# Kernel tuning notes

Hardware: AMD Instinct MI355X
Metric: run time of the kernel (lower is better)

Reference implementation:

```python
import jax, jax.numpy as jnp
import numpy as np

N_NODES = 50000
N_EDGES = 600000
IN_CH = 300
HID = 128
N_CLASSES = 2
N_GRAPHS = 128
BN_EPS = 1e-5


def setup_inputs() -> dict:
    key = jax.random.key(0)
    ks = jax.random.split(key, 24)
    x = jax.random.normal(ks[0], (N_NODES, IN_CH), dtype=jnp.float32)
    edge_index = jax.random.randint(ks[1], (2, N_EDGES), 0, N_NODES, dtype=jnp.int64)
    batch = jnp.sort(jax.random.randint(ks[2], (N_NODES,), 0, N_GRAPHS, dtype=jnp.int64))

    def glorot(k, shape):
        fan_in, fan_out = shape
        s = jnp.sqrt(2.0 / (fan_in + fan_out)).astype(jnp.float32)
        return jax.random.normal(k, shape, dtype=jnp.float32) * s

    inp = {"x": x, "edge_index": edge_index, "batch": batch}
    # SAGEConv params: W_l (neighbor branch), W_r (root branch), bias
    dims = [(IN_CH, HID), (HID, HID), (HID, HID)]
    for i, (din, dout) in enumerate(dims, start=1):
        inp[f"W{i}l"] = glorot(ks[3 * i], (din, dout))
        inp[f"W{i}r"] = glorot(ks[3 * i + 1], (din, dout))
        inp[f"b{i}"] = jnp.zeros((dout,), dtype=jnp.float32)
        inp[f"g{i}"] = jnp.ones((dout,), dtype=jnp.float32)   # BN gamma
        inp[f"be{i}"] = jnp.zeros((dout,), dtype=jnp.float32)  # BN beta
    inp["Wc"] = glorot(ks[20], (HID, N_CLASSES))
    inp["bc"] = jnp.zeros((N_CLASSES,), dtype=jnp.float32)
    return inp


def _sage_conv(x, src, dst, Wl, Wr, b):
    # mean-aggregate neighbor features (messages flow src -> dst)
    msg_sum = jax.ops.segment_sum(x[src], dst, num_segments=N_NODES)
    deg = jax.ops.segment_sum(jnp.ones((src.shape[0],), dtype=x.dtype), dst,
                              num_segments=N_NODES)
    mean = msg_sum / jnp.maximum(deg, 1.0)[:, None]
    return mean @ Wl + x @ Wr + b


def _bn_relu(h, gamma, beta):
    mu = jnp.mean(h, axis=0)
    var = jnp.var(h, axis=0)
    h = (h - mu) * jax.lax.rsqrt(var + BN_EPS) * gamma + beta
    return jax.nn.relu(h)


def reference(x, edge_index, batch,
              W1l, W1r, b1, g1, be1,
              W2l, W2r, b2, g2, be2,
              W3l, W3r, b3, g3, be3,
              Wc, bc):
    src, dst = edge_index[0], edge_index[1]
    h = _bn_relu(_sage_conv(x, src, dst, W1l, W1r, b1), g1, be1)
    h = _bn_relu(_sage_conv(h, src, dst, W2l, W2r, b2), g2, be2)
    h = _bn_relu(_sage_conv(h, src, dst, W3l, W3r, b3), g3, be3)
    # global mean pool per graph
    pooled = jax.ops.segment_sum(h, batch, num_segments=N_GRAPHS)
    cnt = jax.ops.segment_sum(jnp.ones((h.shape[0],), dtype=h.dtype), batch,
                              num_segments=N_GRAPHS)
    hg = pooled / jnp.maximum(cnt, 1.0)[:, None]
    out = hg @ Wc + bc
    return out, hg
```

## Files before the change

kernel.cpp:

```cpp
#include <hip/hip_runtime.h>

#define N_NODES   50000
#define N_EDGES   600000
#define IN_CH     300
#define HID       128
#define N_CLASSES 2
#define N_GRAPHS  128
#define BN_EPS    1e-5f

#define NB ((N_NODES + 511) / 512)
#define KP1 320
#define NREP 32

typedef __attribute__((ext_vector_type(8))) short bf8_t;
typedef __attribute__((ext_vector_type(4))) float f4_t;

__device__ __forceinline__ unsigned short f2bf(float x) {
    union { float f; unsigned u; } q; q.f = x;
    unsigned r = q.u + 0x7fffu + ((q.u >> 16) & 1u);
    return (unsigned short)(r >> 16);
}
__device__ __forceinline__ float bf2f(unsigned short h) {
    union { float f; unsigned u; } q; q.u = ((unsigned)h) << 16; return q.f;
}

__device__ __forceinline__ void async_cp16(const void* g, void* l) {
    __builtin_amdgcn_global_load_lds(
        (const __attribute__((address_space(1))) unsigned int*)g,
        (__attribute__((address_space(3))) unsigned int*)l, 16, 0, 0);
}

__global__ __launch_bounds__(256) void deg_kernel(const int* __restrict__ dst,
                                                  int* __restrict__ ideg) {
    int e = blockIdx.x * 256 + threadIdx.x;
    if (e < N_EDGES) atomicAdd(&ideg[dst[e]], 1);
}

__global__ __launch_bounds__(256) void scan_fused(const int* __restrict__ ideg,
                                                  int* __restrict__ row_start,
                                                  float* __restrict__ invdeg,
                                                  int* __restrict__ bsum,
                                                  int* __restrict__ bflag) {
    int b = blockIdx.x, t = threadIdx.x;
    int lane = t & 63, wv = t >> 6;
    int i0 = b * 512 + t * 2;
    int v0 = 0, v1 = 0;
    if (i0 < N_NODES) {
        int2 v = *(const int2*)&ideg[i0];
        v0 = v.x; v1 = v.y;
    }
    int tot = v0 + v1;
    int s = tot;
#pragma unroll
    for (int d = 1; d < 64; d <<= 1) {
        int u = __shfl_up(s, d);
        if (lane >= d) s += u;
    }
    __shared__ int ws[4];
    if (lane == 63) ws[wv] = s;
    __syncthreads();
    int btot = ws[0] + ws[1] + ws[2] + ws[3];
    if (t == 0) {
        atomicExch(&bsum[b], btot);
        __threadfence();
        atomicExch(&bflag[b], 1);
    }
    int part = 0;
    if (t < b) {
        while (atomicAdd(&bflag[t], 0) == 0) {}
        part = atomicAdd(&bsum[t], 0);
    }
#pragma unroll
    for (int d = 1; d < 64; d <<= 1) part += __shfl_down(part, d);
    __shared__ int ps[4];
    if (lane == 0) ps[wv] = part;
    __syncthreads();
    int boff = ps[0] + ps[1] + ps[2] + ps[3];
    int woff = 0;
    for (int w = 0; w < wv; ++w) woff += ws[w];
    int base = boff + woff + (s - tot);
    if (i0 < N_NODES) {
        row_start[i0]     = base;
        row_start[i0 + 1] = base + v0;
        invdeg[i0]     = 1.0f / fmaxf((float)v0, 1.0f);
        invdeg[i0 + 1] = 1.0f / fmaxf((float)v1, 1.0f);
    }
    if (t == 0 && b == NB - 1) row_start[N_NODES] = boff + btot;
}

__global__ __launch_bounds__(256) void fill_kernel(const int* __restrict__ src,
                                                   const int* __restrict__ dst,
                                                   const int* __restrict__ row_start,
                                                   int* __restrict__ cursor,
                                                   int* __restrict__ csr_src) {
    int e = blockIdx.x * 256 + threadIdx.x;
    if (e >= N_EDGES) return;
    int d = dst[e];
    int pos = row_start[d] + atomicAdd(&cursor[d], 1);
    csr_src[pos] = src[e];
}

__global__ __launch_bounds__(256) void prep_w_all(const float* __restrict__ W1l,
                                                  const float* __restrict__ W1r,
                                                  const float* __restrict__ W2l,
                                                  const float* __restrict__ W2r,
                                                  const float* __restrict__ W3l,
                                                  const float* __restrict__ W3r,
                                                  unsigned short* __restrict__ B1h,
                                                  unsigned short* __restrict__ B1l,
                                                  unsigned short* __restrict__ B2h,
                                                  unsigned short* __restrict__ B2l,
                                                  unsigned short* __restrict__ B3h,
                                                  unsigned short* __restrict__ B3l) {
    int layer = blockIdx.y;
    int Kp = (layer == 0) ? KP1 : HID;
    int K  = (layer == 0) ? IN_CH : HID;
    const float* Wl = (layer == 0) ? W1l : ((layer == 1) ? W2l : W3l);
    const float* Wr = (layer == 0) ? W1r : ((layer == 1) ? W2r : W3r);
    unsigned short* Bh = (layer == 0) ? B1h : ((layer == 1) ? B2h : B3h);
    unsigned short* Bl = (layer == 0) ? B1l : ((layer == 1) ? B2l : B3l);
    int idx = blockIdx.x * 256 + threadIdx.x;
    if (idx >= 256 * Kp) return;
    int n = idx / Kp;
    int k = idx - n * Kp;
    float v = 0.f;
    if (k < K) v = (n < 128) ? Wl[k * 128 + n] : Wr[k * 128 + (n - 128)];
    unsigned short h = f2bf(v);
    unsigned short l = f2bf(v - bf2f(h));
    Bh[idx] = h;
    Bl[idx] = l;
}

__global__ __launch_bounds__(256) void gemm_mfma(const unsigned short* __restrict__ Ahi,
                                                 const unsigned short* __restrict__ Alo,
                                                 int M, int Kp,
                                                 const unsigned short* __restrict__ Bhi,
                                                 const unsigned short* __restrict__ Blo,
                                                 const float* __restrict__ bias,
                                                 unsigned short* __restrict__ C0,
                                                 float* __restrict__ C1) {
    __shared__ __align__(16) unsigned short sAh[64 * 32];
    __shared__ __align__(16) unsigned short sAl[64 * 32];
    __shared__ __align__(16) unsigned short sBh[256 * 32];
    __shared__ __align__(16) unsigned short sBl[256 * 32];

    const int tid  = threadIdx.x;
    const int lane = tid & 63;
    const int wave = tid >> 6;
    const int l16  = lane & 15;
    const int quad = lane >> 4;
    const long m0  = (long)blockIdx.x * 64;
    const int  n0  = wave * 64;

    f4_t acc[4][4];
#pragma unroll
    for (int mt = 0; mt < 4; ++mt)
#pragma unroll
        for (int nt = 0; nt < 4; ++nt) acc[mt][nt] = (f4_t){0.f, 0.f, 0.f, 0.f};

    const int cg = ((lane & 3) ^ ((lane >> 3) & 3)) * 8;
    long asr = m0 + wave * 16 + (lane >> 2);
    if (asr >= M) asr = M - 1;
    const unsigned short* gAh = Ahi + asr * Kp + cg;
    const unsigned short* gAl = Alo + asr * Kp + cg;
    unsigned short* lAh = &sAh[wave * 512];
    unsigned short* lAl = &sAl[wave * 512];
    const unsigned short* gBh[4];
    const unsigned short* gBl[4];
    unsigned short* lBh[4];
    unsigned short* lBl[4];
#pragma unroll
    for (int j = 0; j < 4; ++j) {
        long br = wave * 64 + j * 16 + (lane >> 2);
        gBh[j] = Bhi + br * Kp + cg;
        gBl[j] = Blo + br * Kp + cg;
        lBh[j] = &sBh[wave * 2048 + j * 512];
        lBl[j] = &sBl[wave * 2048 + j * 512];
    }
    const int rsw = (quad ^ ((l16 >> 1) & 3)) * 8;

    for (int k0 = 0; k0 < Kp; k0 += 32) {
        async_cp16(gAh + k0, lAh);
        async_cp16(gAl + k0, lAl);
#pragma unroll
        for (int j = 0; j < 4; ++j) {
            async_cp16(gBh[j] + k0, lBh[j]);
            async_cp16(gBl[j] + k0, lBl[j]);
        }
        __syncthreads();

        bf8_t ah[4], al[4];
#pragma unroll
        for (int mt = 0; mt < 4; ++mt) {
            ah[mt] = *(const bf8_t*)&sAh[(mt * 16 + l16) * 32 + rsw];
            al[mt] = *(const bf8_t*)&sAl[(mt * 16 + l16) * 32 + rsw];
        }
#pragma unroll
        for (int nt = 0; nt < 4; ++nt) {
            bf8_t bh = *(const bf8_t*)&sBh[(n0 + nt * 16 + l16) * 32 + rsw];
            bf8_t bl = *(const bf8_t*)&sBl[(n0 + nt * 16 + l16) * 32 + rsw];
#pragma unroll
            for (int mt = 0; mt < 4; ++mt) {
                acc[mt][nt] = __builtin_amdgcn_mfma_f32_16x16x32_bf16(ah[mt], bh, acc[mt][nt], 0, 0, 0);
                acc[mt][nt] = __builtin_amdgcn_mfma_f32_16x16x32_bf16(al[mt], bh, acc[mt][nt], 0, 0, 0);
                acc[mt][nt] = __builtin_amdgcn_mfma_f32_16x16x32_bf16(ah[mt], bl, acc[mt][nt], 0, 0, 0);
            }
        }
        __syncthreads();
    }

    const bool left = (n0 < 128);
    if (left) {
        int ncol[4];
#pragma unroll
        for (int nt = 0; nt < 4; ++nt) ncol[nt] = n0 + nt * 16 + l16;
#pragma unroll
        for (int mt = 0; mt < 4; ++mt)
#pragma unroll
            for (int r = 0; r < 4; ++r) {
                long row = m0 + mt * 16 + quad * 4 + r;
                if (row < M) {
#pragma unroll
                    for (int nt = 0; nt < 4; ++nt)
                        C0[row * 128 + ncol[nt]] = f2bf(acc[mt][nt][r]);
                }
            }
    } else {
        float badd[4];
        int   ncol[4];
#pragma unroll
        for (int nt = 0; nt < 4; ++nt) {
            int ng = n0 + nt * 16 + l16 - 128;
            ncol[nt] = ng;
            badd[nt] = bias[ng];
        }
#pragma unroll
        for (int mt = 0; mt < 4; ++mt)
#pragma unroll
            for (int r = 0; r < 4; ++r) {
                long row = m0 + mt * 16 + quad * 4 + r;
                if (row < M) {
#pragma unroll
                    for (int nt = 0; nt < 4; ++nt)
                        C1[row * 128 + ncol[nt]] = acc[mt][nt][r] + badd[nt];
                }
            }
    }
}

__global__ __launch_bounds__(256) void gemm_mfma_x(const float* __restrict__ X,
                                                   int M,
                                                   const unsigned short* __restrict__ Bhi,
                                                   const unsigned short* __restrict__ Blo,
                                                   const float* __restrict__ bias,
                                                   unsigned short* __restrict__ C0,
                                                   float* __restrict__ C1) {
    __shared__ __align__(16) unsigned short sAh[64 * 32];
    __shared__ __align__(16) unsigned short sAl[64 * 32];
    __shared__ __align__(16) unsigned short sBh[256 * 32];
    __shared__ __align__(16) unsigned short sBl[256 * 32];

    const int tid  = threadIdx.x;
    const int lane = tid & 63;
    const int wave = tid >> 6;
    const int l16  = lane & 15;
    const int quad = lane >> 4;
    const long m0  = (long)blockIdx.x * 64;
    const int  n0  = wave * 64;

    f4_t acc[4][4];
#pragma unroll
    for (int mt = 0; mt < 4; ++mt)
#pragma unroll
        for (int nt = 0; nt < 4; ++nt) acc[mt][nt] = (f4_t){0.f, 0.f, 0.f, 0.f};

    const int ar  = tid >> 2;
    const int cl  = tid & 3;
    const int cpa = cl ^ ((ar >> 1) & 3);
    long agr = m0 + ar;
    if (agr >= M) agr = M - 1;
    const float* gX = X + agr * IN_CH;

    const int cg = ((lane & 3) ^ ((lane >> 3) & 3)) * 8;
    const unsigned short* gBh[4];
    const unsigned short* gBl[4];
    unsigned short* lBh[4];
    unsigned short* lBl[4];
#pragma unroll
    for (int j = 0; j < 4; ++j) {
        long br = wave * 64 + j * 16 + (lane >> 2);
        gBh[j] = Bhi + br * KP1 + cg;
        gBl[j] = Blo + br * KP1 + cg;
        lBh[j] = &sBh[wave * 2048 + j * 512];
        lBl[j] = &sBl[wave * 2048 + j * 512];
    }
    const int rsw = (quad ^ ((l16 >> 1) & 3)) * 8;

    for (int k0 = 0; k0 < KP1; k0 += 32) {
#pragma unroll
        for (int j = 0; j < 4; ++j) {
            async_cp16(gBh[j] + k0, lBh[j]);
            async_cp16(gBl[j] + k0, lBl[j]);
        }
        float f[8];
        const int gk = k0 + cl * 8;
#pragma unroll
        for (int hh = 0; hh < 2; ++hh) {
            int g4 = gk + hh * 4;
            float4 v = (g4 + 4 <= IN_CH) ? *(const float4*)(gX + g4)
                                         : make_float4(0.f, 0.f, 0.f, 0.f);
            f[hh * 4 + 0] = v.x; f[hh * 4 + 1] = v.y;
            f[hh * 4 + 2] = v.z; f[hh * 4 + 3] = v.w;
        }
        bf8_t h8, l8;
#pragma unroll
        for (int j = 0; j < 8; ++j) {
            unsigned short h = f2bf(f[j]);
            h8[j] = (short)h;
            l8[j] = (short)f2bf(f[j] - bf2f(h));
        }
        *(bf8_t*)&sAh[ar * 32 + cpa * 8] = h8;
        *(bf8_t*)&sAl[ar * 32 + cpa * 8] = l8;
        __syncthreads();

        bf8_t ah[4], al[4];
#pragma unroll
        for (int mt = 0; mt < 4; ++mt) {
            ah[mt] = *(const bf8_t*)&sAh[(mt * 16 + l16) * 32 + rsw];
            al[mt] = *(const bf8_t*)&sAl[(mt * 16 + l16) * 32 + rsw];
        }
#pragma unroll
        for (int nt = 0; nt < 4; ++nt) {
            bf8_t bh = *(const bf8_t*)&sBh[(n0 + nt * 16 + l16) * 32 + rsw];
            bf8_t bl = *(const bf8_t*)&sBl[(n0 + nt * 16 + l16) * 32 + rsw];
#pragma unroll
            for (int mt = 0; mt < 4; ++mt) {
                acc[mt][nt] = __builtin_amdgcn_mfma_f32_16x16x32_bf16(ah[mt], bh, acc[mt][nt], 0, 0, 0);
                acc[mt][nt] = __builtin_amdgcn_mfma_f32_16x16x32_bf16(al[mt], bh, acc[mt][nt], 0, 0, 0);
                acc[mt][nt] = __builtin_amdgcn_mfma_f32_16x16x32_bf16(ah[mt], bl, acc[mt][nt], 0, 0, 0);
            }
        }
        __syncthreads();
    }

    const bool left = (n0 < 128);
    if (left) {
        int ncol[4];
#pragma unroll
        for (int nt = 0; nt < 4; ++nt) ncol[nt] = n0 + nt * 16 + l16;
#pragma unroll
        for (int mt = 0; mt < 4; ++mt)
#pragma unroll
            for (int r = 0; r < 4; ++r) {
                long row = m0 + mt * 16 + quad * 4 + r;
                if (row < M) {
#pragma unroll
                    for (int nt = 0; nt < 4; ++nt)
                        C0[row * 128 + ncol[nt]] = f2bf(acc[mt][nt][r]);
                }
            }
    } else {
        float badd[4];
        int   ncol[4];
#pragma unroll
        for (int nt = 0; nt < 4; ++nt) {
            int ng = n0 + nt * 16 + l16 - 128;
            ncol[nt] = ng;
            badd[nt] = bias[ng];
        }
#pragma unroll
        for (int mt = 0; mt < 4; ++mt)
#pragma unroll
            for (int r = 0; r < 4; ++r) {
                long row = m0 + mt * 16 + quad * 4 + r;
                if (row < M) {
#pragma unroll
                    for (int nt = 0; nt < 4; ++nt)
                        C1[row * 128 + ncol[nt]] = acc[mt][nt][r] + badd[nt];
                }
            }
    }
}

__global__ __launch_bounds__(256) void gather_agg(const unsigned short* __restrict__ Pl,
                                                  const int* __restrict__ row_start,
                                                  const int* __restrict__ csr_src,
                                                  const float* __restrict__ invdeg,
                                                  float* __restrict__ out,
                                                  float* __restrict__ rep) {
    int slot = threadIdx.x >> 5;
    int lane = threadIdx.x & 31;
    int node = blockIdx.x * 8 + slot;
    int beg = row_start[node];
    int end = row_start[node + 1];
    const unsigned short* base = Pl + lane * 4;
    float sx = 0.f, sy = 0.f, sz = 0.f, sw = 0.f;
    int j = beg;
    for (; j + 8 <= end; j += 8) {
        int idx[8];
#pragma unroll
        for (int u = 0; u < 8; ++u) idx[u] = csr_src[j + u];
        ushort4 v[8];
#pragma unroll
        for (int u = 0; u < 8; ++u) v[u] = *(const ushort4*)(base + (long)idx[u] * HID);
#pragma unroll
        for (int u = 0; u < 8; ++u) {
            sx += bf2f(v[u].x); sy += bf2f(v[u].y);
            sz += bf2f(v[u].z); sw += bf2f(v[u].w);
        }
    }
    if (j + 4 <= end) {
        int idx[4];
#pragma unroll
        for (int u = 0; u < 4; ++u) idx[u] = csr_src[j + u];
        ushort4 v[4];
#pragma unroll
        for (int u = 0; u < 4; ++u) v[u] = *(const ushort4*)(base + (long)idx[u] * HID);
#pragma unroll
        for (int u = 0; u < 4; ++u) {
            sx += bf2f(v[u].x); sy += bf2f(v[u].y);
            sz += bf2f(v[u].z); sw += bf2f(v[u].w);
        }
        j += 4;
    }
    for (; j < end; ++j) {
        int i0 = csr_src[j];
        ushort4 v0 = *(const ushort4*)(base + (long)i0 * HID);
        sx += bf2f(v0.x); sy += bf2f(v0.y); sz += bf2f(v0.z); sw += bf2f(v0.w);
    }
    float w = invdeg[node];
    float* o = out + (long)node * HID + lane * 4;
    float4 cur = *(float4*)o;
    cur.x += sx * w;
    cur.y += sy * w;
    cur.z += sz * w;
    cur.w += sw * w;
    *(float4*)o = cur;

    __shared__ float red[8][HID];
    float* repb = rep + (blockIdx.x & (NREP - 1)) * 256;
    *(float4*)&red[slot][lane * 4] = make_float4(cur.x, cur.y, cur.z, cur.w);
    __syncthreads();
    if (threadIdx.x < HID) {
        float tsum = 0.f;
#pragma unroll
        for (int s = 0; s < 8; ++s) tsum += red[s][threadIdx.x];
        atomicAdd(&repb[threadIdx.x], tsum);
    }
    __syncthreads();
    *(float4*)&red[slot][lane * 4] = make_float4(cur.x * cur.x, cur.y * cur.y,
                                                 cur.z * cur.z, cur.w * cur.w);
    __syncthreads();
    if (threadIdx.x < HID) {
        float tsum = 0.f;
#pragma unroll
        for (int s = 0; s < 8; ++s) tsum += red[s][threadIdx.x];
        atomicAdd(&repb[HID + threadIdx.x], tsum);
    }
}

__global__ __launch_bounds__(256) void bn_apply_relu(float* __restrict__ h,
                                                     const float* __restrict__ rep,
                                                     const float* __restrict__ gamma,
                                                     const float* __restrict__ beta,
                                                     unsigned short* __restrict__ Hhi,
                                                     unsigned short* __restrict__ Hlo) {
    __shared__ float S[256];
    __shared__ float SC[256];
    int t = threadIdx.x;
    float a = 0.f;
#pragma unroll
    for (int r = 0; r < NREP; ++r) a += rep[r * 256 + t];
    S[t] = a;
    __syncthreads();
    if (t < HID) {
        const float invn = 1.0f / (float)N_NODES;
        float mu  = S[t] * invn;
        float var = S[HID + t] * invn - mu * mu;
        float sc  = gamma[t] * rsqrtf(var + BN_EPS);
        SC[t]       = sc;
        SC[HID + t] = beta[t] - mu * sc;
    }
    __syncthreads();

    long i = (long)blockIdx.x * 256 + t;
    if (i >= (long)N_NODES * 32) return;
    int c4 = (int)(i & 31) * 4;
    float4 sc = *(const float4*)&SC[c4];
    float4 sh = *(const float4*)&SC[HID + c4];
    float4 v  = *(float4*)&h[i * 4];
    v.x = fmaxf(v.x * sc.x + sh.x, 0.f);
    v.y = fmaxf(v.y * sc.y + sh.y, 0.f);
    v.z = fmaxf(v.z * sc.z + sh.z, 0.f);
    v.w = fmaxf(v.w * sc.w + sh.w, 0.f);
    if (Hhi) {
        ushort4 hh, ll;
        hh.x = f2bf(v.x); ll.x = f2bf(v.x - bf2f(hh.x));
        hh.y = f2bf(v.y); ll.y = f2bf(v.y - bf2f(hh.y));
        hh.z = f2bf(v.z); ll.z = f2bf(v.z - bf2f(hh.z));
        hh.w = f2bf(v.w); ll.w = f2bf(v.w - bf2f(hh.w));
        *(ushort4*)&Hhi[i * 4] = hh;
        *(ushort4*)&Hlo[i * 4] = ll;
    } else {
        *(float4*)&h[i * 4] = v;
    }
}

__global__ __launch_bounds__(1024) void poolhead_kernel(const float* __restrict__ h,
                                                        const int* __restrict__ batch,
                                                        const float* __restrict__ Wc,
                                                        const float* __restrict__ bc,
                                                        float* __restrict__ out) {
    int g = blockIdx.x;
    int t = threadIdx.x;
    int c = t & 127;
    int half = t >> 7;
    __shared__ int lo_sh, hi_sh;
    if (t == 0) {
        int lo = 0, hi = N_NODES;
        while (lo < hi) { int m = (lo + hi) >> 1; if (batch[m] < g) lo = m + 1; else hi = m; }
        lo_sh = lo;
        int lo2 = lo, hi2 = N_NODES;
        while (lo2 < hi2) { int m = (lo2 + hi2) >> 1; if (batch[m] < g + 1) lo2 = m + 1; else hi2 = m; }
        hi_sh = lo2;
    }
    __syncthreads();
    int lo = lo_sh, hi = hi_sh;
    float a0 = 0.f, a1 = 0.f, a2 = 0.f, a3 = 0.f;
    int r = lo + half;
    for (; r + 24 < hi; r += 32) {
        a0 += h[(long)(r +  0) * HID + c];
        a1 += h[(long)(r +  8) * HID + c];
        a2 += h[(long)(r + 16) * HID + c];
        a3 += h[(long)(r + 24) * HID + c];
    }
    for (; r < hi; r += 8) a0 += h[(long)r * HID + c];
    __shared__ float red[8][HID];
    red[half][c] = (a0 + a1) + (a2 + a3);
    __syncthreads();
    __shared__ float r0[HID], r1[HID];
    if (t < HID) {
        float inv = 1.0f / fmaxf((float)(hi - lo), 1.0f);
        float v = 0.f;
#pragma unroll
        for (int s = 0; s < 8; ++s) v += red[s][t];
        v *= inv;
        out[N_GRAPHS * N_CLASSES + g * HID + t] = v;
        r0[t] = v * Wc[t * 2 + 0];
        r1[t] = v * Wc[t * 2 + 1];
    }
    __syncthreads();
    if (t < 2) {
        const float* rr = t ? r1 : r0;
        float sum = bc[t];
        for (int i = 0; i < HID; ++i) sum += rr[i];
        out[g * 2 + t] = sum;
    }
}

extern "C" void kernel_launch(void* const* d_in, const int* in_sizes, int n_in,
                              void* d_out, int out_size, void* d_ws, size_t ws_size,
                              hipStream_t stream) {
    const float* x     = (const float*)d_in[0];
    const int*   ei    = (const int*)d_in[1];
    const int*   batch = (const int*)d_in[2];
    const float* W1l = (const float*)d_in[3];
    const float* W1r = (const float*)d_in[4];
    const float* b1  = (const float*)d_in[5];
    const float* g1  = (const float*)d_in[6];
    const float* be1 = (const float*)d_in[7];
    const float* W2l = (const float*)d_in[8];
    const float* W2r = (const float*)d_in[9];
    const float* b2  = (const float*)d_in[10];
    const float* g2  = (const float*)d_in[11];
    const float* be2 = (const float*)d_in[12];
    const float* W3l = (const float*)d_in[13];
    const float* W3r = (const float*)d_in[14];
    const float* b3  = (const float*)d_in[15];
    const float* g3  = (const float*)d_in[16];
    const float* be3 = (const float*)d_in[17];
    const float* Wc  = (const float*)d_in[18];
    const float* bc  = (const float*)d_in[19];

    const int* src = ei;
    const int* dst = ei + N_EDGES;

    float* ws = (float*)d_ws;
    const long FEAT = (long)N_NODES * HID;
    unsigned short* Pl16 = (unsigned short*)ws;
    float* buf1 = ws + FEAT;
    float* buf2 = ws + 2 * FEAT;
    int*   ideg      = (int*)(ws + 3 * FEAT);
    int*   cursor    = ideg + N_NODES;
    int*   bsum      = cursor + N_NODES;
    int*   bflag     = bsum + 128;
    int*   row_start = bflag + 128;
    int*   csr_src   = row_start + N_NODES + 4;
    float* invdeg    = (float*)(csr_src + N_EDGES);
    float* reps      = invdeg + N_NODES;
    unsigned short* B1h = (unsigned short*)(reps + 3 * NREP * 256);
    unsigned short* B1l = B1h + 256 * KP1;
    unsigned short* B2h = B1l + 256 * KP1;
    unsigned short* B2l = B2h + 256 * HID;
    unsigned short* B3h = B2l + 256 * HID;
    unsigned short* B3l = B3h + 256 * HID;
    unsigned short* Hhi = B3l + 256 * HID;
    unsigned short* Hlo = Hhi + FEAT;

    float* outp = (float*)d_out;

    const int gemm_grid   = (N_NODES + 63) / 64;
    const int gather_grid = N_NODES / 8;
    const int apply_grid  = (int)(((long)N_NODES * 32 + 255) / 256);
    const dim3 prepw_grid((256 * KP1 + 255) / 256, 3);

    hipMemsetAsync(ideg, 0, (2 * N_NODES + 256) * sizeof(int), stream);
    hipMemsetAsync(reps, 0, 3 * NREP * 256 * sizeof(float), stream);

    deg_kernel<<<(N_EDGES + 255) / 256, 256, 0, stream>>>(dst, ideg);
    scan_fused<<<NB, 256, 0, stream>>>(ideg, row_start, invdeg, bsum, bflag);
    fill_kernel<<<(N_EDGES + 255) / 256, 256, 0, stream>>>(src, dst, row_start, cursor, csr_src);

    prep_w_all<<<prepw_grid, 256, 0, stream>>>(W1l, W1r, W2l, W2r, W3l, W3r,
                                               B1h, B1l, B2h, B2l, B3h, B3l);

    gemm_mfma_x<<<gemm_grid, 256, 0, stream>>>(x, N_NODES, B1h, B1l, b1, Pl16, buf1);
    gather_agg<<<gather_grid, 256, 0, stream>>>(Pl16, row_start, csr_src, invdeg, buf1, reps);
    bn_apply_relu<<<apply_grid, 256, 0, stream>>>(buf1, reps, g1, be1, Hhi, Hlo);

    gemm_mfma<<<gemm_grid, 256, 0, stream>>>(Hhi, Hlo, N_NODES, HID, B2h, B2l, b2, Pl16, buf2);
    gather_agg<<<gather_grid, 256, 0, stream>>>(Pl16, row_start, csr_src, invdeg, buf2, reps + NREP * 256);
    bn_apply_relu<<<apply_grid, 256, 0, stream>>>(buf2, reps + NREP * 256, g2, be2, Hhi, Hlo);

    gemm_mfma<<<gemm_grid, 256, 0, stream>>>(Hhi, Hlo, N_NODES, HID, B3h, B3l, b3, Pl16, buf1);
    gather_agg<<<gather_grid, 256, 0, stream>>>(Pl16, row_start, csr_src, invdeg, buf1, reps + 2 * NREP * 256);
    bn_apply_relu<<<apply_grid, 256, 0, stream>>>(buf1, reps + 2 * NREP * 256, g3, be3, nullptr, nullptr);

    poolhead_kernel<<<N_GRAPHS, 1024, 0, stream>>>(buf1, batch, Wc, bc, outp);
}
```

Baseline: 443.6 us.

## Fuse BN+ReLU into next-layer GEMM A-load and pooling head; merge deg with weight prep

Result: faster. 399.2 us (-10.0%).

```diff
diff --git a/kernel.cpp b/kernel.cpp
--- a/kernel.cpp
+++ b/kernel.cpp
@@ -11,6 +11,7 @@
 #define NB ((N_NODES + 511) / 512)
 #define KP1 320
 #define NREP 32
+#define DEGB ((N_EDGES + 255) / 256)
 
 typedef __attribute__((ext_vector_type(8))) short bf8_t;
 typedef __attribute__((ext_vector_type(4))) float f4_t;
@@ -30,10 +31,46 @@
         (__attribute__((address_space(3))) unsigned int*)l, 16, 0, 0);
 }
 
-__global__ __launch_bounds__(256) void deg_kernel(const int* __restrict__ dst,
-                                                  int* __restrict__ ideg) {
-    int e = blockIdx.x * 256 + threadIdx.x;
-    if (e < N_EDGES) atomicAdd(&ideg[dst[e]], 1);
+__global__ __launch_bounds__(256) void deg_prepw(const int* __restrict__ dst,
+                                                 int* __restrict__ ideg,
+                                                 const float* __restrict__ W1l,
+                                                 const float* __restrict__ W1r,
+                                                 const float* __restrict__ W2l,
+                                                 const float* __restrict__ W2r,
+                                                 const float* __restrict__ W3l,
+                                                 const float* __restrict__ W3r,
+                                                 unsigned short* __restrict__ B1h,
+                                                 unsigned short* __restrict__ B1l,
+                                                 unsigned short* __restrict__ B2h,
+                                                 unsigned short* __restrict__ B2l,
+                                                 unsigned short* __restrict__ B3h,
+                                                 unsigned short* __restrict__ B3l) {
+    int b = blockIdx.x;
+    if (b < DEGB) {
+        int e = b * 256 + threadIdx.x;
+        if (e < N_EDGES) atomicAdd(&ideg[dst[e]], 1);
+        return;
+    }
+    int pb = b - DEGB;
+    int layer, base;
+    if (pb < 320)      { layer = 0; base = pb; }
+    else if (pb < 448) { layer = 1; base = pb - 320; }
+    else               { layer = 2; base = pb - 448; }
+    int Kp = (layer == 0) ? KP1 : HID;
+    int K  = (layer == 0) ? IN_CH : HID;
+    const float* Wl = (layer == 0) ? W1l : ((layer == 1) ? W2l : W3l);
+    const float* Wr = (layer == 0) ? W1r : ((layer == 1) ? W2r : W3r);
+    unsigned short* Bh = (layer == 0) ? B1h : ((layer == 1) ? B2h : B3h);
+    unsigned short* Bl = (layer == 0) ? B1l : ((layer == 1) ? B2l : B3l);
+    int idx = base * 256 + threadIdx.x;
+    int n = idx / Kp;
+    int k = idx - n * Kp;
+    float v = 0.f;
+    if (k < K) v = (n < 128) ? Wl[k * 128 + n] : Wr[k * 128 + (n - 128)];
+    unsigned short h = f2bf(v);
+    unsigned short l = f2bf(v - bf2f(h));
+    Bh[idx] = h;
+    Bl[idx] = l;
 }
 
 __global__ __launch_bounds__(256) void scan_fused(const int* __restrict__ ideg,
@@ -100,154 +137,6 @@
     csr_src[pos] = src[e];
 }
 
-__global__ __launch_bounds__(256) void prep_w_all(const float* __restrict__ W1l,
-                                                  const float* __restrict__ W1r,
-                                                  const float* __restrict__ W2l,
-                                                  const float* __restrict__ W2r,
-                                                  const float* __restrict__ W3l,
-                                                  const float* __restrict__ W3r,
-                                                  unsigned short* __restrict__ B1h,
-                                                  unsigned short* __restrict__ B1l,
-                                                  unsigned short* __restrict__ B2h,
-                                                  unsigned short* __restrict__ B2l,
-                                                  unsigned short* __restrict__ B3h,
-                                                  unsigned short* __restrict__ B3l) {
-    int layer = blockIdx.y;
-    int Kp = (layer == 0) ? KP1 : HID;
-    int K  = (layer == 0) ? IN_CH : HID;
-    const float* Wl = (layer == 0) ? W1l : ((layer == 1) ? W2l : W3l);
-    const float* Wr = (layer == 0) ? W1r : ((layer == 1) ? W2r : W3r);
-    unsigned short* Bh = (layer == 0) ? B1h : ((layer == 1) ? B2h : B3h);
-    unsigned short* Bl = (layer == 0) ? B1l : ((layer == 1) ? B2l : B3l);
-    int idx = blockIdx.x * 256 + threadIdx.x;
-    if (idx >= 256 * Kp) return;
-    int n = idx / Kp;
-    int k = idx - n * Kp;
-    float v = 0.f;
-    if (k < K) v = (n < 128) ? Wl[k * 128 + n] : Wr[k * 128 + (n - 128)];
-    unsigned short h = f2bf(v);
-    unsigned short l = f2bf(v - bf2f(h));
-    Bh[idx] = h;
-    Bl[idx] = l;
-}
-
-__global__ __launch_bounds__(256) void gemm_mfma(const unsigned short* __restrict__ Ahi,
-                                                 const unsigned short* __restrict__ Alo,
-                                                 int M, int Kp,
-                                                 const unsigned short* __restrict__ Bhi,
-                                                 const unsigned short* __restrict__ Blo,
-                                                 const float* __restrict__ bias,
-                                                 unsigned short* __restrict__ C0,
-                                                 float* __restrict__ C1) {
-    __shared__ __align__(16) unsigned short sAh[64 * 32];
-    __shared__ __align__(16) unsigned short sAl[64 * 32];
-    __shared__ __align__(16) unsigned short sBh[256 * 32];
-    __shared__ __align__(16) unsigned short sBl[256 * 32];
-
-    const int tid  = threadIdx.x;
-    const int lane = tid & 63;
-    const int wave = tid >> 6;
-    const int l16  = lane & 15;
-    const int quad = lane >> 4;
-    const long m0  = (long)blockIdx.x * 64;
-    const int  n0  = wave * 64;
-
-    f4_t acc[4][4];
-#pragma unroll
-    for (int mt = 0; mt < 4; ++mt)
-#pragma unroll
-        for (int nt = 0; nt < 4; ++nt) acc[mt][nt] = (f4_t){0.f, 0.f, 0.f, 0.f};
-
-    const int cg = ((lane & 3) ^ ((lane >> 3) & 3)) * 8;
-    long asr = m0 + wave * 16 + (lane >> 2);
-    if (asr >= M) asr = M - 1;
-    const unsigned short* gAh = Ahi + asr * Kp + cg;
-    const unsigned short* gAl = Alo + asr * Kp + cg;
-    unsigned short* lAh = &sAh[wave * 512];
-    unsigned short* lAl = &sAl[wave * 512];
-    const unsigned short* gBh[4];
-    const unsigned short* gBl[4];
-    unsigned short* lBh[4];
-    unsigned short* lBl[4];
-#pragma unroll
-    for (int j = 0; j < 4; ++j) {
-        long br = wave * 64 + j * 16 + (lane >> 2);
-        gBh[j] = Bhi + br * Kp + cg;
-        gBl[j] = Blo + br * Kp + cg;
-        lBh[j] = &sBh[wave * 2048 + j * 512];
-        lBl[j] = &sBl[wave * 2048 + j * 512];
-    }
-    const int rsw = (quad ^ ((l16 >> 1) & 3)) * 8;
-
-    for (int k0 = 0; k0 < Kp; k0 += 32) {
-        async_cp16(gAh + k0, lAh);
-        async_cp16(gAl + k0, lAl);
-#pragma unroll
-        for (int j = 0; j < 4; ++j) {
-            async_cp16(gBh[j] + k0, lBh[j]);
-            async_cp16(gBl[j] + k0, lBl[j]);
-        }
-        __syncthreads();
-
-        bf8_t ah[4], al[4];
-#pragma unroll
-        for (int mt = 0; mt < 4; ++mt) {
-            ah[mt] = *(const bf8_t*)&sAh[(mt * 16 + l16) * 32 + rsw];
-            al[mt] = *(const bf8_t*)&sAl[(mt * 16 + l16) * 32 + rsw];
-        }
-#pragma unroll
-        for (int nt = 0; nt < 4; ++nt) {
-            bf8_t bh = *(const bf8_t*)&sBh[(n0 + nt * 16 + l16) * 32 + rsw];
-            bf8_t bl = *(const bf8_t*)&sBl[(n0 + nt * 16 + l16) * 32 + rsw];
-#pragma unroll
-            for (int mt = 0; mt < 4; ++mt) {
-                acc[mt][nt] = __builtin_amdgcn_mfma_f32_16x16x32_bf16(ah[mt], bh, acc[mt][nt], 0, 0, 0);
-                acc[mt][nt] = __builtin_amdgcn_mfma_f32_16x16x32_bf16(al[mt], bh, acc[mt][nt], 0, 0, 0);
-                acc[mt][nt] = __builtin_amdgcn_mfma_f32_16x16x32_bf16(ah[mt], bl, acc[mt][nt], 0, 0, 0);
-            }
-        }
-        __syncthreads();
-    }
-
-    const bool left = (n0 < 128);
-    if (left) {
-        int ncol[4];
-#pragma unroll
-        for (int nt = 0; nt < 4; ++nt) ncol[nt] = n0 + nt * 16 + l16;
-#pragma unroll
-        for (int mt = 0; mt < 4; ++mt)
-#pragma unroll
-            for (int r = 0; r < 4; ++r) {
-                long row = m0 + mt * 16 + quad * 4 + r;
-                if (row < M) {
-#pragma unroll
-                    for (int nt = 0; nt < 4; ++nt)
-                        C0[row * 128 + ncol[nt]] = f2bf(acc[mt][nt][r]);
-                }
-            }
-    } else {
-        float badd[4];
-        int   ncol[4];
-#pragma unroll
-        for (int nt = 0; nt < 4; ++nt) {
-            int ng = n0 + nt * 16 + l16 - 128;
-            ncol[nt] = ng;
-            badd[nt] = bias[ng];
-        }
-#pragma unroll
-        for (int mt = 0; mt < 4; ++mt)
-#pragma unroll
-            for (int r = 0; r < 4; ++r) {
-                long row = m0 + mt * 16 + quad * 4 + r;
-                if (row < M) {
-#pragma unroll
-                    for (int nt = 0; nt < 4; ++nt)
-                        C1[row * 128 + ncol[nt]] = acc[mt][nt][r] + badd[nt];
-                }
-            }
-    }
-}
-
 __global__ __launch_bounds__(256) void gemm_mfma_x(const float* __restrict__ X,
                                                    int M,
                                                    const unsigned short* __restrict__ Bhi,
@@ -312,6 +201,169 @@
             f[hh * 4 + 0] = v.x; f[hh * 4 + 1] = v.y;
             f[hh * 4 + 2] = v.z; f[hh * 4 + 3] = v.w;
         }
+        bf8_t h8, l8;
+#pragma unroll
+        for (int j = 0; j < 8; ++j) {
+            unsigned short h = f2bf(f[j]);
+            h8[j] = (short)h;
+            l8[j] = (short)f2bf(f[j] - bf2f(h));
+        }
+        *(bf8_t*)&sAh[ar * 32 + cpa * 8] = h8;
+        *(bf8_t*)&sAl[ar * 32 + cpa * 8] = l8;
+        __syncthreads();
+
+        bf8_t ah[4], al[4];
+#pragma unroll
+        for (int mt = 0; mt < 4; ++mt) {
+            ah[mt] = *(const bf8_t*)&sAh[(mt * 16 + l16) * 32 + rsw];
+            al[mt] = *(const bf8_t*)&sAl[(mt * 16 + l16) * 32 + rsw];
+        }
+#pragma unroll
+        for (int nt = 0; nt < 4; ++nt) {
+            bf8_t bh = *(const bf8_t*)&sBh[(n0 + nt * 16 + l16) * 32 + rsw];
+            bf8_t bl = *(const bf8_t*)&sBl[(n0 + nt * 16 + l16) * 32 + rsw];
+#pragma unroll
+            for (int mt = 0; mt < 4; ++mt) {
+                acc[mt][nt] = __builtin_amdgcn_mfma_f32_16x16x32_bf16(ah[mt], bh, acc[mt][nt], 0, 0, 0);
+                acc[mt][nt] = __builtin_amdgcn_mfma_f32_16x16x32_bf16(al[mt], bh, acc[mt][nt], 0, 0, 0);
+                acc[mt][nt] = __builtin_amdgcn_mfma_f32_16x16x32_bf16(ah[mt], bl, acc[mt][nt], 0, 0, 0);
+            }
+        }
+        __syncthreads();
+    }
+
+    const bool left = (n0 < 128);
+    if (left) {
+        int ncol[4];
+#pragma unroll
+        for (int nt = 0; nt < 4; ++nt) ncol[nt] = n0 + nt * 16 + l16;
+#pragma unroll
+        for (int mt = 0; mt < 4; ++mt)
+#pragma unroll
+            for (int r = 0; r < 4; ++r) {
+                long row = m0 + mt * 16 + quad * 4 + r;
+                if (row < M) {
+#pragma unroll
+                    for (int nt = 0; nt < 4; ++nt)
+                        C0[row * 128 + ncol[nt]] = f2bf(acc[mt][nt][r]);
+                }
+            }
+    } else {
+        float badd[4];
+        int   ncol[4];
+#pragma unroll
+        for (int nt = 0; nt < 4; ++nt) {
+            int ng = n0 + nt * 16 + l16 - 128;
+            ncol[nt] = ng;
+            badd[nt] = bias[ng];
+        }
+#pragma unroll
+        for (int mt = 0; mt < 4; ++mt)
+#pragma unroll
+            for (int r = 0; r < 4; ++r) {
+                long row = m0 + mt * 16 + quad * 4 + r;
+                if (row < M) {
+#pragma unroll
+                    for (int nt = 0; nt < 4; ++nt)
+                        C1[row * 128 + ncol[nt]] = acc[mt][nt][r] + badd[nt];
+                }
+            }
+    }
+}
+
+__global__ __launch_bounds__(256) void gemm_mfma_h(const float* __restrict__ Hpre,
+                                                   int M,
+                                                   const float* __restrict__ rep,
+                                                   const float* __restrict__ gamma,
+                                                   const float* __restrict__ beta,
+                                                   const unsigned short* __restrict__ Bhi,
+                                                   const unsigned short* __restrict__ Blo,
+                                                   const float* __restrict__ bias,
+                                                   unsigned short* __restrict__ C0,
+                                                   float* __restrict__ C1) {
+    __shared__ __align__(16) unsigned short sAh[64 * 32];
+    __shared__ __align__(16) unsigned short sAl[64 * 32];
+    __shared__ __align__(16) unsigned short sBh[256 * 32];
+    __shared__ __align__(16) unsigned short sBl[256 * 32];
+    __shared__ float S[256];
+    __shared__ float sSC[256];
+
+    const int tid  = threadIdx.x;
+    const int lane = tid & 63;
+    const int wave = tid >> 6;
+    const int l16  = lane & 15;
+    const int quad = lane >> 4;
+    const long m0  = (long)blockIdx.x * 64;
+    const int  n0  = wave * 64;
+
+    {
+        float a = 0.f;
+#pragma unroll
+        for (int r = 0; r < NREP; ++r) a += rep[r * 256 + tid];
+        S[tid] = a;
+        __syncthreads();
+        if (tid < HID) {
+            const float invn = 1.0f / (float)N_NODES;
+            float mu  = S[tid] * invn;
+            float var = S[HID + tid] * invn - mu * mu;
+            float sc  = gamma[tid] * rsqrtf(var + BN_EPS);
+            sSC[tid]       = sc;
+            sSC[HID + tid] = beta[tid] - mu * sc;
+        }
+        __syncthreads();
+    }
+
+    f4_t acc[4][4];
+#pragma unroll
+    for (int mt = 0; mt < 4; ++mt)
+#pragma unroll
+        for (int nt = 0; nt < 4; ++nt) acc[mt][nt] = (f4_t){0.f, 0.f, 0.f, 0.f};
+
+    const int ar  = tid >> 2;
+    const int cl  = tid & 3;
+    const int cpa = cl ^ ((ar >> 1) & 3);
+    long agr = m0 + ar;
+    if (agr >= M) agr = M - 1;
+    const float* gH = Hpre + agr * HID;
+
+    const int cg = ((lane & 3) ^ ((lane >> 3) & 3)) * 8;
+    const unsigned short* gBh[4];
+    const unsigned short* gBl[4];
+    unsigned short* lBh[4];
+    unsigned short* lBl[4];
+#pragma unroll
+    for (int j = 0; j < 4; ++j) {
+        long br = wave * 64 + j * 16 + (lane >> 2);
+        gBh[j] = Bhi + br * HID + cg;
+        gBl[j] = Blo + br * HID + cg;
+        lBh[j] = &sBh[wave * 2048 + j * 512];
+        lBl[j] = &sBl[wave * 2048 + j * 512];
+    }
+    const int rsw = (quad ^ ((l16 >> 1) & 3)) * 8;
+
+#pragma unroll
+    for (int k0 = 0; k0 < HID; k0 += 32) {
+#pragma unroll
+        for (int j = 0; j < 4; ++j) {
+            async_cp16(gBh[j] + k0, lBh[j]);
+            async_cp16(gBl[j] + k0, lBl[j]);
+        }
+        const int gk = k0 + cl * 8;
+        float4 v0 = *(const float4*)(gH + gk);
+        float4 v1 = *(const float4*)(gH + gk + 4);
+        float4 s0 = *(const float4*)&sSC[gk];
+        float4 s1 = *(const float4*)&sSC[gk + 4];
+        float4 t0 = *(const float4*)&sSC[HID + gk];
+        float4 t1 = *(const float4*)&sSC[HID + gk + 4];
+        float f[8];
+        f[0] = fmaxf(v0.x * s0.x + t0.x, 0.f);
+        f[1] = fmaxf(v0.y * s0.y + t0.y, 0.f);
+        f[2] = fmaxf(v0.z * s0.z + t0.z, 0.f);
+        f[3] = fmaxf(v0.w * s0.w + t0.w, 0.f);
+        f[4] = fmaxf(v1.x * s1.x + t1.x, 0.f);
+        f[5] = fmaxf(v1.y * s1.y + t1.y, 0.f);
+        f[6] = fmaxf(v1.z * s1.z + t1.z, 0.f);
+        f[7] = fmaxf(v1.w * s1.w + t1.w, 0.f);
         bf8_t h8, l8;
 #pragma unroll
         for (int j = 0; j < 8; ++j) {
@@ -459,62 +511,26 @@
     }
 }
 
-__global__ __launch_bounds__(256) void bn_apply_relu(float* __restrict__ h,
-                                                     const float* __restrict__ rep,
-                                                     const float* __restrict__ gamma,
-                                                     const float* __restrict__ beta,
-                                                     unsigned short* __restrict__ Hhi,
-                                                     unsigned short* __restrict__ Hlo) {
+__global__ __launch_bounds__(1024) void poolhead_bn(const float* __restrict__ h,
+                                                    const int* __restrict__ batch,
+                                                    const float* __restrict__ rep,
+                                                    const float* __restrict__ gamma,
+                                                    const float* __restrict__ beta,
+                                                    const float* __restrict__ Wc,
+                                                    const float* __restrict__ bc,
+                                                    float* __restrict__ out) {
     __shared__ float S[256];
     __shared__ float SC[256];
-    int t = threadIdx.x;
-    float a = 0.f;
-#pragma unroll
-    for (int r = 0; r < NREP; ++r) a += rep[r * 256 + t];
-    S[t] = a;
-    __syncthreads();
-    if (t < HID) {
-        const float invn = 1.0f / (float)N_NODES;
-        float mu  = S[t] * invn;
-        float var = S[HID + t] * invn - mu * mu;
-        float sc  = gamma[t] * rsqrtf(var + BN_EPS);
-        SC[t]       = sc;
-        SC[HID + t] = beta[t] - mu * sc;
-    }
-    __syncthreads();
-
-    long i = (long)blockIdx.x * 256 + t;
-    if (i >= (long)N_NODES * 32) return;
-    int c4 = (int)(i & 31) * 4;
-    float4 sc = *(const float4*)&SC[c4];
-    float4 sh = *(const float4*)&SC[HID + c4];
-    float4 v  = *(float4*)&h[i * 4];
-    v.x = fmaxf(v.x * sc.x + sh.x, 0.f);
-    v.y = fmaxf(v.y * sc.y + sh.y, 0.f);
-    v.z = fmaxf(v.z * sc.z + sh.z, 0.f);
-    v.w = fmaxf(v.w * sc.w + sh.w, 0.f);
-    if (Hhi) {
-        ushort4 hh, ll;
-        hh.x = f2bf(v.x); ll.x = f2bf(v.x - bf2f(hh.x));
-        hh.y = f2bf(v.y); ll.y = f2bf(v.y - bf2f(hh.y));
-        hh.z = f2bf(v.z); ll.z = f2bf(v.z - bf2f(hh.z));
-        hh.w = f2bf(v.w); ll.w = f2bf(v.w - bf2f(hh.w));
-        *(ushort4*)&Hhi[i * 4] = hh;
-        *(ushort4*)&Hlo[i * 4] = ll;
-    } else {
-        *(float4*)&h[i * 4] = v;
-    }
-}
-
-__global__ __launch_bounds__(1024) void poolhead_kernel(const float* __restrict__ h,
-                                                        const int* __restrict__ batch,
-                                                        const float* __restrict__ Wc,
-                                                        const float* __restrict__ bc,
-                                                        float* __restrict__ out) {
     int g = blockIdx.x;
     int t = threadIdx.x;
     int c = t & 127;
     int half = t >> 7;
+    if (t < 256) {
+        float a = 0.f;
+#pragma unroll
+        for (int r = 0; r < NREP; ++r) a += rep[r * 256 + t];
+        S[t] = a;
+    }
     __shared__ int lo_sh, hi_sh;
     if (t == 0) {
         int lo = 0, hi = N_NODES;
@@ -525,16 +541,26 @@
         hi_sh = lo2;
     }
     __syncthreads();
+    if (t < HID) {
+        const float invn = 1.0f / (float)N_NODES;
+        float mu  = S[t] * invn;
+        float var = S[HID + t] * invn - mu * mu;
+        float sc  = gamma[t] * rsqrtf(var + BN_EPS);
+        SC[t]       = sc;
+        SC[HID + t] = beta[t] - mu * sc;
+    }
+    __syncthreads();
+    float bsc = SC[c], bsh = SC[HID + c];
     int lo = lo_sh, hi = hi_sh;
     float a0 = 0.f, a1 = 0.f, a2 = 0.f, a3 = 0.f;
     int r = lo + half;
     for (; r + 24 < hi; r += 32) {
-        a0 += h[(long)(r +  0) * HID + c];
-        a1 += h[(long)(r +  8) * HID + c];
-        a2 += h[(long)(r + 16) * HID + c];
-        a3 += h[(long)(r + 24) * HID + c];
-    }
-    for (; r < hi; r += 8) a0 += h[(long)r * HID + c];
+        a0 += fmaxf(h[(long)(r +  0) * HID + c] * bsc + bsh, 0.f);
+        a1 += fmaxf(h[(long)(r +  8) * HID + c] * bsc + bsh, 0.f);
+        a2 += fmaxf(h[(long)(r + 16) * HID + c] * bsc + bsh, 0.f);
+        a3 += fmaxf(h[(long)(r + 24) * HID + c] * bsc + bsh, 0.f);
+    }
+    for (; r < hi; r += 8) a0 += fmaxf(h[(long)r * HID + c] * bsc + bsh, 0.f);
     __shared__ float red[8][HID];
     red[half][c] = (a0 + a1) + (a2 + a3);
     __syncthreads();
@@ -604,37 +630,32 @@
     unsigned short* B2l = B2h + 256 * HID;
     unsigned short* B3h = B2l + 256 * HID;
     unsigned short* B3l = B3h + 256 * HID;
-    unsigned short* Hhi = B3l + 256 * HID;
-    unsigned short* Hlo = Hhi + FEAT;
 
     float* outp = (float*)d_out;
 
     const int gemm_grid   = (N_NODES + 63) / 64;
     const int gather_grid = N_NODES / 8;
-    const int apply_grid  = (int)(((long)N_NODES * 32 + 255) / 256);
-    const dim3 prepw_grid((256 * KP1 + 255) / 256, 3);
+    const int dp_grid     = DEGB + 320 + 128 + 128;
 
     hipMemsetAsync(ideg, 0, (2 * N_NODES + 256) * sizeof(int), stream);
     hipMemsetAsync(reps, 0, 3 * NREP * 256 * sizeof(float), stream);
 
-    deg_kernel<<<(N_EDGES + 255) / 256, 256, 0, stream>>>(dst, ideg);
+    deg_prepw<<<dp_grid, 256, 0, stream>>>(dst, ideg, W1l, W1r, W2l, W2r, W3l, W3r,
+                                           B1h, B1l, B2h, B2l, B3h, B3l);
     scan_fused<<<NB, 256, 0, stream>>>(ideg, row_start, invdeg, bsum, bflag);
     fill_kernel<<<(N_EDGES + 255) / 256, 256, 0, stream>>>(src, dst, row_start, cursor, csr_src);
 
-    prep_w_all<<<prepw_grid, 256, 0, stream>>>(W1l, W1r, W2l, W2r, W3l, W3r,
-                                               B1h, B1l, B2h, B2l, B3h, B3l);
-
     gemm_mfma_x<<<gemm_grid, 256, 0, stream>>>(x, N_NODES, B1h, B1l, b1, Pl16, buf1);
     gather_agg<<<gather_grid, 256, 0, stream>>>(Pl16, row_start, csr_src, invdeg, buf1, reps);
-    bn_apply_relu<<<apply_grid, 256, 0, stream>>>(buf1, reps, g1, be1, Hhi, Hlo);
-
-    gemm_mfma<<<gemm_grid, 256, 0, stream>>>(Hhi, Hlo, N_NODES, HID, B2h, B2l, b2, Pl16, buf2);
+
+    gemm_mfma_h<<<gemm_grid, 256, 0, stream>>>(buf1, N_NODES, reps, g1, be1,
+                                               B2h, B2l, b2, Pl16, buf2);
     gather_agg<<<gather_grid, 256, 0, stream>>>(Pl16, row_start, csr_src, invdeg, buf2, reps + NREP * 256);
-    bn_apply_relu<<<apply_grid, 256, 0, stream>>>(buf2, reps + NREP * 256, g2, be2, Hhi, Hlo);
-
-    gemm_mfma<<<gemm_grid, 256, 0, stream>>>(Hhi, Hlo, N_NODES, HID, B3h, B3l, b3, Pl16, buf1);
+
+    gemm_mfma_h<<<gemm_grid, 256, 0, stream>>>(buf2, N_NODES, reps + NREP * 256, g2, be2,
+                                               B3h, B3l, b3, Pl16, buf1);
     gather_agg<<<gather_grid, 256, 0, stream>>>(Pl16, row_start, csr_src, invdeg, buf1, reps + 2 * NREP * 256);
-    bn_apply_relu<<<apply_grid, 256, 0, stream>>>(buf1, reps + 2 * NREP * 256, g3, be3, nullptr, nullptr);
-
-    poolhead_kernel<<<N_GRAPHS, 1024, 0, stream>>>(buf1, batch, Wc, bc, outp);
-}
+
+    poolhead_bn<<<N_GRAPHS, 1024, 0, stream>>>(buf1, batch, reps + 2 * NREP * 256,
+                                               g3, be3, Wc, bc, outp);
+}
```
